# Optimization experiments

Measured on AMD Instinct MI355X. Metric: run time of the kernel, lower is better.

## Reference

```python
import jax, jax.numpy as jnp
import numpy as np

TAU_M = 5.0 / 3.0
V_TH = 1.0


def setup_inputs() -> dict:
    key = jax.random.key(0)
    T, B, C, H, W = 8, 32, 128, 32, 32
    x = jax.random.normal(key, (T, B, C, H, W), dtype=jnp.float32)
    return {"x": x}


def reference(x):
    """LIF neuron: leaky integrate, bidirectional threshold fire (+1/-1), hard reset.
    x: [T, B, C, H, W]. Returns spike train output: [T, B, C, H, W]."""
    def step(V, x_t):
        dv = -V / TAU_M + x_t          # leak + input current
        V_new = V + dv                  # integrate
        out = (V_new >= V_TH).astype(x_t.dtype) - (V_new <= -V_TH).astype(x_t.dtype)
        V_next = (1.0 - jnp.abs(out)) * V_new   # reset to 0 where spiked
        return V_next, out

    V0 = jnp.zeros_like(x[0])
    _, output = jax.lax.scan(step, V0, x)
    return output
```

## Files before the change

kernel.cpp:

```cpp
#include <hip/hip_runtime.h>


#define T_STEPS 8

typedef float vfloat4 __attribute__((ext_vector_type(4)));

struct StepOut { float V; float o; };

__device__ __forceinline__ StepOut lif_step(float V, float x) {
    const float TAU = (float)(5.0 / 3.0);
    float dv = (-V) / TAU + x;
    float Vn = V + dv;
    float o = (Vn >= 1.0f ? 1.0f : 0.0f) - (Vn <= -1.0f ? 1.0f : 0.0f);
    StepOut r;
    r.o = o;
    r.V = (o == 0.0f) ? Vn : 0.0f;
    return r;
}

__device__ __forceinline__ vfloat4 lif_step4(vfloat4& V, vfloat4 xt) {
    StepOut a = lif_step(V.x, xt.x);
    StepOut b = lif_step(V.y, xt.y);
    StepOut c = lif_step(V.z, xt.z);
    StepOut d = lif_step(V.w, xt.w);
    vfloat4 Vn, o;
    Vn.x = a.V; Vn.y = b.V; Vn.z = c.V; Vn.w = d.V;
    o.x = a.o;  o.y = b.o;  o.z = c.o;  o.w = d.o;
    V = Vn;
    return o;
}

__global__ __launch_bounds__(256) void lif_kernel(const vfloat4* __restrict__ x,
                                                  vfloat4* __restrict__ out,
                                                  int n4) {
    const int Q = n4 >> 2;
    int q = blockIdx.x * blockDim.x + threadIdx.x;
    if (q >= Q) return;

    const size_t s = (size_t)n4;
    const size_t i0 = (size_t)q;
    const size_t i1 = (size_t)q + (size_t)Q;
    const size_t i2 = (size_t)q + 2 * (size_t)Q;
    const size_t i3 = (size_t)q + 3 * (size_t)Q;

    vfloat4 Va = (vfloat4)(0.f);
    vfloat4 Vb = Va, Vc = Va, Vd = Va;

#pragma unroll
    for (int t = 0; t < T_STEPS; ++t) {
        const size_t base = (size_t)t * s;
        vfloat4 xa = __builtin_nontemporal_load(&x[base + i0]);
        vfloat4 xb = __builtin_nontemporal_load(&x[base + i1]);
        vfloat4 xc = __builtin_nontemporal_load(&x[base + i2]);
        vfloat4 xd = __builtin_nontemporal_load(&x[base + i3]);

        vfloat4 oa = lif_step4(Va, xa);
        vfloat4 ob = lif_step4(Vb, xb);
        vfloat4 oc = lif_step4(Vc, xc);
        vfloat4 od = lif_step4(Vd, xd);

        __builtin_nontemporal_store(oa, &out[base + i0]);
        __builtin_nontemporal_store(ob, &out[base + i1]);
        __builtin_nontemporal_store(oc, &out[base + i2]);
        __builtin_nontemporal_store(od, &out[base + i3]);
    }
}

extern "C" void kernel_launch(void* const* d_in, const int* in_sizes, int n_in,
                              void* d_out, int out_size, void* d_ws, size_t ws_size,
                              hipStream_t stream) {
    const float* x = (const float*)d_in[0];
    float* out = (float*)d_out;

    int total = in_sizes[0];
    int n = total / T_STEPS;
    int n4 = n / 4;
    int Q = n4 / 4;

    dim3 block(256);
    dim3 grid((Q + block.x - 1) / block.x);
    lif_kernel<<<grid, block, 0, stream>>>((const vfloat4*)x, (vfloat4*)out, n4);
}
```

Measured before the change: 221.4 us.

## Split LIF into pack kernel with 2-bit spike codes and parallel unpack kernel

Splits the LIF scan into two kernels. The first reads the inputs, runs the recurrence and writes 2-bit spike codes for all time steps into a workspace. The second kernel launches four times as many threads, each expanding the codes into float outputs. This spreads the write-heavy phase over more threads to raise memory parallelism, at the cost of an extra launch and a small workspace round-trip. If the workspace is too small, the original single-kernel path is used.

```diff
diff --git a/kernel.cpp b/kernel.cpp
--- a/kernel.cpp
+++ b/kernel.cpp
@@ -4,6 +4,7 @@
 #define T_STEPS 8
 
 typedef float vfloat4 __attribute__((ext_vector_type(4)));
+typedef unsigned long long u64;
 
 struct StepOut { float V; float o; };
 
@@ -30,9 +31,21 @@
     return o;
 }
 
-__global__ __launch_bounds__(256) void lif_kernel(const vfloat4* __restrict__ x,
-                                                  vfloat4* __restrict__ out,
-                                                  int n4) {
+__device__ __forceinline__ unsigned enc(float o) {
+    return (o == 1.0f) ? 1u : ((o == -1.0f) ? 2u : 0u);
+}
+
+__device__ __forceinline__ unsigned enc4(vfloat4 o) {
+    return enc(o.x) | (enc(o.y) << 2) | (enc(o.z) << 4) | (enc(o.w) << 6);
+}
+
+__device__ __forceinline__ float dec(unsigned c) {
+    return (c == 1u) ? 1.0f : ((c == 2u) ? -1.0f : 0.0f);
+}
+
+__global__ __launch_bounds__(256) void lif_pack(const vfloat4* __restrict__ x,
+                                                u64* __restrict__ ws,
+                                                int n4) {
     const int Q = n4 >> 2;
     int q = blockIdx.x * blockDim.x + threadIdx.x;
     if (q >= Q) return;
@@ -45,6 +58,7 @@
 
     vfloat4 Va = (vfloat4)(0.f);
     vfloat4 Vb = Va, Vc = Va, Vd = Va;
+    u64 pa = 0, pb = 0, pc = 0, pd = 0;
 
 #pragma unroll
     for (int t = 0; t < T_STEPS; ++t) {
@@ -59,6 +73,61 @@
         vfloat4 oc = lif_step4(Vc, xc);
         vfloat4 od = lif_step4(Vd, xd);
 
+        pa |= ((u64)enc4(oa)) << (8 * t);
+        pb |= ((u64)enc4(ob)) << (8 * t);
+        pc |= ((u64)enc4(oc)) << (8 * t);
+        pd |= ((u64)enc4(od)) << (8 * t);
+    }
+    __builtin_nontemporal_store(pa, &ws[i0]);
+    __builtin_nontemporal_store(pb, &ws[i1]);
+    __builtin_nontemporal_store(pc, &ws[i2]);
+    __builtin_nontemporal_store(pd, &ws[i3]);
+}
+
+__global__ __launch_bounds__(256) void lif_unpack(const u64* __restrict__ ws,
+                                                  vfloat4* __restrict__ out,
+                                                  int n4) {
+    int i = blockIdx.x * blockDim.x + threadIdx.x;
+    if (i >= n4) return;
+
+    u64 u = __builtin_nontemporal_load(&ws[i]);
+    const size_t s = (size_t)n4;
+#pragma unroll
+    for (int t = 0; t < T_STEPS; ++t) {
+        unsigned byte = (unsigned)(u >> (8 * t)) & 0xFFu;
+        vfloat4 o;
+        o.x = dec(byte & 3u);
+        o.y = dec((byte >> 2) & 3u);
+        o.z = dec((byte >> 4) & 3u);
+        o.w = dec((byte >> 6) & 3u);
+        __builtin_nontemporal_store(o, &out[(size_t)t * s + i]);
+    }
+}
+
+__global__ __launch_bounds__(256) void lif_single(const vfloat4* __restrict__ x,
+                                                  vfloat4* __restrict__ out,
+                                                  int n4) {
+    const int Q = n4 >> 2;
+    int q = blockIdx.x * blockDim.x + threadIdx.x;
+    if (q >= Q) return;
+    const size_t s = (size_t)n4;
+    const size_t i0 = (size_t)q;
+    const size_t i1 = (size_t)q + (size_t)Q;
+    const size_t i2 = (size_t)q + 2 * (size_t)Q;
+    const size_t i3 = (size_t)q + 3 * (size_t)Q;
+    vfloat4 Va = (vfloat4)(0.f);
+    vfloat4 Vb = Va, Vc = Va, Vd = Va;
+#pragma unroll
+    for (int t = 0; t < T_STEPS; ++t) {
+        const size_t base = (size_t)t * s;
+        vfloat4 xa = __builtin_nontemporal_load(&x[base + i0]);
+        vfloat4 xb = __builtin_nontemporal_load(&x[base + i1]);
+        vfloat4 xc = __builtin_nontemporal_load(&x[base + i2]);
+        vfloat4 xd = __builtin_nontemporal_load(&x[base + i3]);
+        vfloat4 oa = lif_step4(Va, xa);
+        vfloat4 ob = lif_step4(Vb, xb);
+        vfloat4 oc = lif_step4(Vc, xc);
+        vfloat4 od = lif_step4(Vd, xd);
         __builtin_nontemporal_store(oa, &out[base + i0]);
         __builtin_nontemporal_store(ob, &out[base + i1]);
         __builtin_nontemporal_store(oc, &out[base + i2]);
@@ -77,7 +146,17 @@
     int n4 = n / 4;
     int Q = n4 / 4;
 
+    size_t need = (size_t)n4 * sizeof(u64);
     dim3 block(256);
-    dim3 grid((Q + block.x - 1) / block.x);
-    lif_kernel<<<grid, block, 0, stream>>>((const vfloat4*)x, (vfloat4*)out, n4);
+
+    if (ws_size >= need) {
+        dim3 gridP((Q + block.x - 1) / block.x);
+        dim3 gridU((n4 + block.x - 1) / block.x);
+        u64* ws = (u64*)d_ws;
+        lif_pack<<<gridP, block, 0, stream>>>((const vfloat4*)x, ws, n4);
+        lif_unpack<<<gridU, block, 0, stream>>>(ws, (vfloat4*)out, n4);
+    } else {
+        dim3 grid1((Q + block.x - 1) / block.x);
+        lif_single<<<grid1, block, 0, stream>>>((const vfloat4*)x, (vfloat4*)out, n4);
+    }
 }
```

Result: slower. 232.7 us (+5.1%).
